# Kernel optimization log

Hardware: AMD Instinct MI355X
Metric: run time of the kernel (lower is better)

The kernel has to match this reference:

```python
import jax, jax.numpy as jnp
import numpy as np
from jax import lax

WINDOW = 40          # plan.window_size
E = 8                # len(plan.expand_feature)
F = 64               # len(plan.feature)
OUT_CH = 128
KERNEL = 5
ALPHA = 0.01         # leaky_relu_alpha
N_LABEL = 1


def time_conv(x, conv_size):
    """x: [N, T, F] -> [N, WINDOW, 5*E] sliding-window stats over first E features."""
    N, T, _ = x.shape
    begin = T - (conv_size + WINDOW - 1)
    xe = x[:, :, :E]                                             # [N, T, E]
    idx = begin + jnp.arange(WINDOW)[:, None] + jnp.arange(conv_size)[None, :]  # [W, C]
    win = xe[:, idx, :]                                          # [N, W, C, E]
    _mean = win.mean(axis=2)                                     # [N, W, E]
    _std = jnp.std(win, axis=2, ddof=1)                          # torch.std is unbiased
    _max = win.max(axis=2)
    _min = win.min(axis=2)
    # rank of last timestep of each window, cross-sectionally over stocks (dim 0)
    last = xe[:, begin + conv_size - 1: begin + conv_size - 1 + WINDOW, :]  # [N, W, E]
    order = jnp.argsort(-last, axis=0)
    rank = jnp.argsort(order, axis=0).astype(x.dtype) / N        # [N, W, E]
    return jnp.concatenate([_mean, _std, rank, _max, _min], axis=2)  # [N, W, 5E]


def setup_inputs() -> dict:
    key = jax.random.key(0)
    k1, k2, k3, k4, k5 = jax.random.split(key, 5)
    N, T = 8000, 64
    in_ch = F + 10 * E  # 144
    x = jax.random.normal(k1, (N, T, F), dtype=jnp.float32)
    conv_w = jax.random.normal(k2, (OUT_CH, in_ch, KERNEL), dtype=jnp.float32) * 0.05
    conv_b = jax.random.normal(k3, (OUT_CH,), dtype=jnp.float32) * 0.05
    lin_in = WINDOW + 1 - KERNEL  # 36
    lin_w = jax.random.normal(k4, (N_LABEL, lin_in), dtype=jnp.float32) * 0.1
    lin_b = jax.random.normal(k5, (N_LABEL,), dtype=jnp.float32) * 0.1
    return {"x": x, "conv_w": conv_w, "conv_b": conv_b, "lin_w": lin_w, "lin_b": lin_b}


def reference(x, conv_w, conv_b, lin_w, lin_b):
    week_x = time_conv(x, conv_size=5)     # [N, W, 5E]
    month_x = time_conv(x, conv_size=20)   # [N, W, 5E]
    xc = jnp.concatenate([x[:, -WINDOW:, :], week_x, month_x], axis=2)  # [N, W, F+10E]
    cnn_x = jnp.transpose(xc, (0, 2, 1))   # [N, C, W]
    part = lax.conv_general_dilated(cnn_x, conv_w, window_strides=(1,),
                                    padding='VALID',
                                    dimension_numbers=('NCH', 'OIH', 'NCH'))
    part = part + conv_b[None, :, None]    # [N, OUT_CH, W+1-K]
    h = part[:, -1, :]                     # last output channel, [N, W+1-K]
    h = jnp.where(h >= 0, h, ALPHA * h)    # leaky relu
    return h @ lin_w.T + lin_b             # [N, N_LABEL]
```

## Files before the change

### kernel.cpp

```cpp
#include <hip/hip_runtime.h>
#include <math.h>

#define NS    8000
#define TT    64
#define FF    64
#define EE    8
#define WIN   40
#define TR    59
#define NBINS 1024

#define XET_SZ  (8*59*8000)
#define RNK_SZ  (8*40*8000)
#define UDER_SZ (40*5*8000)

__global__ __launch_bounds__(256) void k_transpose(const float* __restrict__ x,
                                                   float* __restrict__ xeT) {
    int n = blockIdx.x * 256 + threadIdx.x;
    int r = blockIdx.y;
    if (n >= NS) return;
    const float* row = x + (size_t)n * (TT * FF) + (5 + r) * FF;
    float4 a = *(const float4*)(row);
    float4 b = *(const float4*)(row + 4);
    xeT[(0 * TR + r) * NS + n] = a.x;
    xeT[(1 * TR + r) * NS + n] = a.y;
    xeT[(2 * TR + r) * NS + n] = a.z;
    xeT[(3 * TR + r) * NS + n] = a.w;
    xeT[(4 * TR + r) * NS + n] = b.x;
    xeT[(5 * TR + r) * NS + n] = b.y;
    xeT[(6 * TR + r) * NS + n] = b.z;
    xeT[(7 * TR + r) * NS + n] = b.w;
}

__device__ __forceinline__ int binOf(float v) {
    int b = (int)((v + 4.0f) * 128.0f);
    b = b < 0 ? 0 : b;
    return b > (NBINS - 1) ? (NBINS - 1) : b;
}

__global__ __launch_bounds__(1024) void k_rank(const float* __restrict__ xeT,
                                               float* __restrict__ rankT) {
    const int w = blockIdx.x;
    const int e = blockIdx.y;
    __shared__ unsigned hist[NBINS];
    __shared__ unsigned basev[NBINS];
    __shared__ unsigned bendv[NBINS];
    __shared__ float          sk[NS];
    __shared__ unsigned short si[NS];
    __shared__ unsigned wsum[16];

    const int tid  = threadIdx.x;
    const int lane = tid & 63;
    const int wid  = tid >> 6;
    const float* col = xeT + ((size_t)e * TR + (19 + w)) * NS;

    float val[8];
#pragma unroll
    for (int i = 0; i < 8; i++) {
        int idx = tid + i * 1024;
        val[i] = (idx < NS) ? col[idx] : 0.0f;
    }
    hist[tid] = 0;
    __syncthreads();

#pragma unroll
    for (int i = 0; i < 8; i++) {
        int idx = tid + i * 1024;
        if (idx < NS) atomicAdd(&hist[binOf(val[i])], 1u);
    }
    __syncthreads();

    unsigned h = hist[tid];
    unsigned sc = h;
#pragma unroll
    for (int d = 1; d < 64; d <<= 1) {
        unsigned t2 = __shfl_up(sc, d);
        if (lane >= d) sc += t2;
    }
    if (lane == 63) wsum[wid] = sc;
    __syncthreads();
    unsigned woff = 0;
    for (int i = 0; i < wid; i++) woff += wsum[i];
    unsigned before = woff + (sc - h);
    bendv[tid] = NS - before;
    basev[tid] = NS - before - h;
    hist[tid]  = NS - before - h;
    __syncthreads();

#pragma unroll
    for (int i = 0; i < 8; i++) {
        int idx = tid + i * 1024;
        if (idx < NS) {
            int b = binOf(val[i]);
            unsigned p = atomicAdd(&hist[b], 1u);
            sk[p] = val[i];
            si[p] = (unsigned short)idx;
        }
    }
    __syncthreads();

    float* outp = rankT + ((size_t)e * WIN + w) * NS;
#pragma unroll 1
    for (int i = 0; i < 8; i++) {
        int p = tid + i * 1024;
        if (p < NS) {
            float v = sk[p];
            unsigned idm = si[p];
            int b = binOf(v);
            unsigned lo = basev[b], hi = bendv[b];
            unsigned c = 0;
            for (unsigned q = lo; q < hi; q++) {
                float u2 = sk[q];
                c += (u2 > v) || (u2 == v && si[q] < idm);
            }
            outp[idm] = (float)(basev[b] + c) / 8000.0f;
        }
    }
}

__global__ __launch_bounds__(256) void k_raw(const float* __restrict__ x,
                                             const float* __restrict__ cw,
                                             float* __restrict__ uraw) {
    const int n    = blockIdx.x * 4 + (threadIdx.x >> 6);
    const int lane = threadIdx.x & 63;
    const int g    = lane >> 4;
    const int l    = lane & 15;
    const float* W = cw + 127 * 144 * 5;

    float wreg[20];
    {
        const float4* Wq = (const float4*)(W + l * 20);
#pragma unroll
        for (int q = 0; q < 5; q++) {
            float4 t = Wq[q];
            wreg[q * 4 + 0] = t.x; wreg[q * 4 + 1] = t.y;
            wreg[q * 4 + 2] = t.z; wreg[q * 4 + 3] = t.w;
        }
    }

    const float* xbase = x + (size_t)n * (TT * FF) + 24 * FF + l * 4;
    float* ubase = uraw + (size_t)n * (WIN * 5);

#pragma unroll 1
    for (int w0 = 0; w0 < WIN; w0 += 4) {
        const int w = w0 + g;
        float4 xv = *(const float4*)(xbase + w * FF);
        float acc[5];
#pragma unroll
        for (int k = 0; k < 5; k++) {
            acc[k] = xv.x * wreg[0 * 5 + k] + xv.y * wreg[1 * 5 + k]
                   + xv.z * wreg[2 * 5 + k] + xv.w * wreg[3 * 5 + k];
        }
#pragma unroll
        for (int d = 1; d < 16; d <<= 1) {
#pragma unroll
            for (int k = 0; k < 5; k++) acc[k] += __shfl_xor(acc[k], d, 64);
        }
        if (l < 5) {
            float v = acc[0];
            if (l == 1) v = acc[1];
            else if (l == 2) v = acc[2];
            else if (l == 3) v = acc[3];
            else if (l == 4) v = acc[4];
            ubase[w * 5 + l] = v;
        }
    }
}

__global__ __launch_bounds__(256) void k_der(const float* __restrict__ cw,
                                             const float* __restrict__ xeT,
                                             const float* __restrict__ rankT,
                                             float* __restrict__ uder) {
    const int n = blockIdx.x * 256 + threadIdx.x;
    const int w = blockIdx.y;
    if (n >= NS) return;
    const float* W = cw + 127 * 144 * 5;

    float g[5] = {0.f, 0.f, 0.f, 0.f, 0.f};

    for (int e = 0; e < 8; e++) {
        const float* colbase = xeT + ((size_t)e * TR + w) * NS + n;
        float xv[20];
#pragma unroll
        for (int j = 0; j < 20; j++) xv[j] = colbase[(size_t)j * NS];

        float s20 = 0.f, mn20 = xv[0], mx20 = xv[0];
#pragma unroll
        for (int i = 0; i < 20; i++) {
            float v = xv[i];
            s20 += v; mn20 = fminf(mn20, v); mx20 = fmaxf(mx20, v);
        }
        float m20 = s20 * (1.0f / 20.0f);
        float d20 = 0.f;
#pragma unroll
        for (int i = 0; i < 20; i++) { float t = xv[i] - m20; d20 += t * t; }
        float sd20 = sqrtf(d20 * (1.0f / 19.0f));

        float s5 = 0.f, mn5 = xv[15], mx5 = xv[15];
#pragma unroll
        for (int i = 15; i < 20; i++) {
            float v = xv[i];
            s5 += v; mn5 = fminf(mn5, v); mx5 = fmaxf(mx5, v);
        }
        float m5 = s5 * 0.2f;
        float d5 = 0.f;
#pragma unroll
        for (int i = 15; i < 20; i++) { float t = xv[i] - m5; d5 += t * t; }
        float sd5 = sqrtf(d5 * 0.25f);

        float rk = rankT[((size_t)e * WIN + w) * NS + n];

#pragma unroll
        for (int k = 0; k < 5; k++) {
            float uk;
            uk  = m5   * W[(64  + e) * 5 + k];
            uk += sd5  * W[(72  + e) * 5 + k];
            uk += rk   * (W[(80 + e) * 5 + k] + W[(120 + e) * 5 + k]);
            uk += mx5  * W[(88  + e) * 5 + k];
            uk += mn5  * W[(96  + e) * 5 + k];
            uk += m20  * W[(104 + e) * 5 + k];
            uk += sd20 * W[(112 + e) * 5 + k];
            uk += mx20 * W[(128 + e) * 5 + k];
            uk += mn20 * W[(136 + e) * 5 + k];
            g[k] += uk;
        }
    }

#pragma unroll
    for (int k = 0; k < 5; k++)
        uder[(size_t)(w * 5 + k) * NS + n] = g[k];
}

__global__ __launch_bounds__(256) void k_final(const float* __restrict__ uraw,
                                               const float* __restrict__ uder,
                                               const float* __restrict__ cb,
                                               const float* __restrict__ lw,
                                               const float* __restrict__ lb,
                                               float* __restrict__ outp) {
    int n = blockIdx.x * 256 + threadIdx.x;
    if (n >= NS) return;
    float b127 = cb[127];
    float acc = lb[0];
    const float* ur = uraw + (size_t)n * (WIN * 5);
#pragma unroll
    for (int j = 0; j < 36; j++) {
        float g = b127;
#pragma unroll
        for (int k = 0; k < 5; k++) {
            int c = (j + k) * 5 + k;
            g += ur[c] + uder[(size_t)c * NS + n];
        }
        g = (g >= 0.0f) ? g : 0.01f * g;
        acc += g * lw[j];
    }
    outp[n] = acc;
}

extern "C" void kernel_launch(void* const* d_in, const int* in_sizes, int n_in,
                              void* d_out, int out_size, void* d_ws, size_t ws_size,
                              hipStream_t stream) {
    const float* x  = (const float*)d_in[0];
    const float* cw = (const float*)d_in[1];
    const float* cb = (const float*)d_in[2];
    const float* lw = (const float*)d_in[3];
    const float* lb = (const float*)d_in[4];
    float* outp = (float*)d_out;

    float* ws    = (float*)d_ws;
    float* xeT   = ws;
    float* rankT = ws + XET_SZ;
    float* uder  = ws + XET_SZ + RNK_SZ;
    float* uraw  = ws + XET_SZ + RNK_SZ + UDER_SZ;

    k_transpose<<<dim3(32, 59), 256, 0, stream>>>(x, xeT);
    k_rank<<<dim3(WIN, EE), 1024, 0, stream>>>(xeT, rankT);
    k_raw<<<2000, 256, 0, stream>>>(x, cw, uraw);
    k_der<<<dim3(32, WIN), 256, 0, stream>>>(cw, xeT, rankT, uder);
    k_final<<<32, 256, 0, stream>>>(uraw, uder, cb, lw, lb, outp);
}
```

Before: 269.6 us.

## Fuse derived-feature and final kernels with sliding ring buffer; double rank histogram bins

The derived-feature kernel and the final reduction are merged into one kernel. Each thread now owns one (stock, expand feature) pair and slides a 20-element ring buffer over time, so xeT is loaded once per row rather than 20 times. Per-feature partial sums are reduced across the 8 features in shared memory, and the uder intermediate buffer with its global round-trip goes away. Separately, the rank histogram doubles to 2048 bins to shrink bucket sizes in the counting sort. The trade-offs are a 36-element per-thread accumulator plus a 20-element ring, which adds register pressure, and only 250 blocks in the fused launch, which lowers parallelism.

```diff
diff --git a/kernel.cpp b/kernel.cpp
--- a/kernel.cpp
+++ b/kernel.cpp
@@ -7,11 +7,10 @@
 #define EE    8
 #define WIN   40
 #define TR    59
-#define NBINS 1024
+#define NBINS 2048
 
 #define XET_SZ  (8*59*8000)
 #define RNK_SZ  (8*40*8000)
-#define UDER_SZ (40*5*8000)
 
 __global__ __launch_bounds__(256) void k_transpose(const float* __restrict__ x,
                                                    float* __restrict__ xeT) {
@@ -32,7 +31,7 @@
 }
 
 __device__ __forceinline__ int binOf(float v) {
-    int b = (int)((v + 4.0f) * 128.0f);
+    int b = (int)((v + 4.0f) * 256.0f);
     b = b < 0 ? 0 : b;
     return b > (NBINS - 1) ? (NBINS - 1) : b;
 }
@@ -60,6 +59,7 @@
         val[i] = (idx < NS) ? col[idx] : 0.0f;
     }
     hist[tid] = 0;
+    hist[tid + 1024] = 0;
     __syncthreads();
 
 #pragma unroll
@@ -69,8 +69,10 @@
     }
     __syncthreads();
 
-    unsigned h = hist[tid];
-    unsigned sc = h;
+    unsigned h0 = hist[2 * tid + 0];
+    unsigned h1 = hist[2 * tid + 1];
+    unsigned cs = h0 + h1;
+    unsigned sc = cs;
 #pragma unroll
     for (int d = 1; d < 64; d <<= 1) {
         unsigned t2 = __shfl_up(sc, d);
@@ -80,10 +82,14 @@
     __syncthreads();
     unsigned woff = 0;
     for (int i = 0; i < wid; i++) woff += wsum[i];
-    unsigned before = woff + (sc - h);
-    bendv[tid] = NS - before;
-    basev[tid] = NS - before - h;
-    hist[tid]  = NS - before - h;
+    unsigned before = woff + (sc - cs);
+    {
+        int b = 2 * tid;
+        bendv[b] = NS - before; before += h0; basev[b] = NS - before;
+        hist[b] = basev[b];  b++;
+        bendv[b] = NS - before; before += h1; basev[b] = NS - before;
+        hist[b] = basev[b];
+    }
     __syncthreads();
 
 #pragma unroll
@@ -166,93 +172,110 @@
     }
 }
 
-__global__ __launch_bounds__(256) void k_der(const float* __restrict__ cw,
-                                             const float* __restrict__ xeT,
-                                             const float* __restrict__ rankT,
-                                             float* __restrict__ uder) {
-    const int n = blockIdx.x * 256 + threadIdx.x;
-    const int w = blockIdx.y;
-    if (n >= NS) return;
+__global__ __launch_bounds__(256) void k_der_final(const float* __restrict__ cw,
+                                                   const float* __restrict__ xeT,
+                                                   const float* __restrict__ rankT,
+                                                   const float* __restrict__ uraw,
+                                                   const float* __restrict__ cb,
+                                                   const float* __restrict__ lw,
+                                                   const float* __restrict__ lb,
+                                                   float* __restrict__ outp) {
+    __shared__ float red[8][32][37];
+    const int tid = threadIdx.x;
+    const int e   = tid >> 5;
+    const int nl  = tid & 31;
+    const int n0  = blockIdx.x * 32;
+    const int n   = n0 + nl;
     const float* W = cw + 127 * 144 * 5;
 
-    float g[5] = {0.f, 0.f, 0.f, 0.f, 0.f};
-
-    for (int e = 0; e < 8; e++) {
-        const float* colbase = xeT + ((size_t)e * TR + w) * NS + n;
-        float xv[20];
-#pragma unroll
-        for (int j = 0; j < 20; j++) xv[j] = colbase[(size_t)j * NS];
-
-        float s20 = 0.f, mn20 = xv[0], mx20 = xv[0];
+    float gder[36];
+#pragma unroll
+    for (int j = 0; j < 36; j++) gder[j] = 0.0f;
+
+    const float* col = xeT + (size_t)e * TR * NS + n;
+    const float* rkp = rankT + (size_t)e * WIN * NS + n;
+
+    float ring[20];
+#pragma unroll
+    for (int r = 0; r < 19; r++) ring[r] = col[(size_t)r * NS];
+
+#pragma unroll
+    for (int w = 0; w < WIN; w++) {
+        ring[(w + 19) % 20] = col[(size_t)(w + 19) * NS];
+        float s20 = 0.f, mn20 = ring[0], mx20 = ring[0];
 #pragma unroll
         for (int i = 0; i < 20; i++) {
-            float v = xv[i];
+            float v = ring[i];
             s20 += v; mn20 = fminf(mn20, v); mx20 = fmaxf(mx20, v);
         }
         float m20 = s20 * (1.0f / 20.0f);
         float d20 = 0.f;
 #pragma unroll
-        for (int i = 0; i < 20; i++) { float t = xv[i] - m20; d20 += t * t; }
+        for (int i = 0; i < 20; i++) { float t = ring[i] - m20; d20 += t * t; }
         float sd20 = sqrtf(d20 * (1.0f / 19.0f));
 
-        float s5 = 0.f, mn5 = xv[15], mx5 = xv[15];
+        float s5 = 0.f, mn5 = ring[(w + 15) % 20], mx5 = mn5;
 #pragma unroll
         for (int i = 15; i < 20; i++) {
-            float v = xv[i];
+            float v = ring[(w + i) % 20];
             s5 += v; mn5 = fminf(mn5, v); mx5 = fmaxf(mx5, v);
         }
         float m5 = s5 * 0.2f;
         float d5 = 0.f;
 #pragma unroll
-        for (int i = 15; i < 20; i++) { float t = xv[i] - m5; d5 += t * t; }
+        for (int i = 15; i < 20; i++) {
+            float t = ring[(w + i) % 20] - m5; d5 += t * t;
+        }
         float sd5 = sqrtf(d5 * 0.25f);
 
-        float rk = rankT[((size_t)e * WIN + w) * NS + n];
+        float rk = rkp[(size_t)w * NS];
 
 #pragma unroll
         for (int k = 0; k < 5; k++) {
-            float uk;
-            uk  = m5   * W[(64  + e) * 5 + k];
-            uk += sd5  * W[(72  + e) * 5 + k];
-            uk += rk   * (W[(80 + e) * 5 + k] + W[(120 + e) * 5 + k]);
-            uk += mx5  * W[(88  + e) * 5 + k];
-            uk += mn5  * W[(96  + e) * 5 + k];
-            uk += m20  * W[(104 + e) * 5 + k];
-            uk += sd20 * W[(112 + e) * 5 + k];
-            uk += mx20 * W[(128 + e) * 5 + k];
-            uk += mn20 * W[(136 + e) * 5 + k];
-            g[k] += uk;
-        }
-    }
-
-#pragma unroll
-    for (int k = 0; k < 5; k++)
-        uder[(size_t)(w * 5 + k) * NS + n] = g[k];
-}
-
-__global__ __launch_bounds__(256) void k_final(const float* __restrict__ uraw,
-                                               const float* __restrict__ uder,
-                                               const float* __restrict__ cb,
-                                               const float* __restrict__ lw,
-                                               const float* __restrict__ lb,
-                                               float* __restrict__ outp) {
-    int n = blockIdx.x * 256 + threadIdx.x;
-    if (n >= NS) return;
-    float b127 = cb[127];
-    float acc = lb[0];
-    const float* ur = uraw + (size_t)n * (WIN * 5);
-#pragma unroll
-    for (int j = 0; j < 36; j++) {
-        float g = b127;
-#pragma unroll
-        for (int k = 0; k < 5; k++) {
-            int c = (j + k) * 5 + k;
-            g += ur[c] + uder[(size_t)c * NS + n];
-        }
-        g = (g >= 0.0f) ? g : 0.01f * g;
-        acc += g * lw[j];
-    }
-    outp[n] = acc;
+            int j = w - k;
+            if (j >= 0 && j < 36) {
+                float uk;
+                uk  = m5   * W[(64  + e) * 5 + k];
+                uk += sd5  * W[(72  + e) * 5 + k];
+                uk += rk   * (W[(80 + e) * 5 + k] + W[(120 + e) * 5 + k]);
+                uk += mx5  * W[(88  + e) * 5 + k];
+                uk += mn5  * W[(96  + e) * 5 + k];
+                uk += m20  * W[(104 + e) * 5 + k];
+                uk += sd20 * W[(112 + e) * 5 + k];
+                uk += mx20 * W[(128 + e) * 5 + k];
+                uk += mn20 * W[(136 + e) * 5 + k];
+                gder[j] += uk;
+            }
+        }
+    }
+
+#pragma unroll
+    for (int j = 0; j < 36; j++) red[e][nl][j] = gder[j];
+    __syncthreads();
+
+    for (int p = tid; p < 32 * 36; p += 256) {
+        int nl2 = p / 36, j = p - nl2 * 36;
+        float sum = 0.f;
+#pragma unroll
+        for (int e2 = 0; e2 < 8; e2++) sum += red[e2][nl2][j];
+        red[0][nl2][j] = sum;
+    }
+    __syncthreads();
+
+    if (tid < 32) {
+        const float* ur = uraw + (size_t)n * (WIN * 5);
+        float b127 = cb[127];
+        float acc = lb[0];
+#pragma unroll
+        for (int j = 0; j < 36; j++) {
+            float g = b127 + red[0][tid][j];
+#pragma unroll
+            for (int k = 0; k < 5; k++) g += ur[(j + k) * 5 + k];
+            g = (g >= 0.0f) ? g : 0.01f * g;
+            acc += g * lw[j];
+        }
+        outp[n] = acc;
+    }
 }
 
 extern "C" void kernel_launch(void* const* d_in, const int* in_sizes, int n_in,
@@ -268,12 +291,10 @@
     float* ws    = (float*)d_ws;
     float* xeT   = ws;
     float* rankT = ws + XET_SZ;
-    float* uder  = ws + XET_SZ + RNK_SZ;
-    float* uraw  = ws + XET_SZ + RNK_SZ + UDER_SZ;
+    float* uraw  = ws + XET_SZ + RNK_SZ;
 
     k_transpose<<<dim3(32, 59), 256, 0, stream>>>(x, xeT);
     k_rank<<<dim3(WIN, EE), 1024, 0, stream>>>(xeT, rankT);
     k_raw<<<2000, 256, 0, stream>>>(x, cw, uraw);
-    k_der<<<dim3(32, WIN), 256, 0, stream>>>(cw, xeT, rankT, uder);
-    k_final<<<32, 256, 0, stream>>>(uraw, uder, cb, lw, lb, outp);
-}
+    k_der_final<<<250, 256, 0, stream>>>(cw, xeT, rankT, uraw, cb, lw, lb, outp);
+}
```

Result: faster. 253.0 us (-6.2%).
